# Kernel optimization log

Measured on AMD Instinct MI355X. Metric: run time of the kernel, lower is better.

Reference implementation:

```python
import jax, jax.numpy as jnp
import numpy as np

ND, NPR, DD, DP, LAT, AT, B = 2048, 2048, 128, 128, 128, 32, 16384


def setup_inputs():
    key = jax.random.key(0)
    ks = jax.random.split(key, 20)
    s = 0.05
    d = {}
    d["e_p_adj"] = (jax.random.uniform(ks[0], (ND, NPR)) < 0.05).astype(jnp.float32)
    d["e_e_adj"] = (jax.random.uniform(ks[1], (ND, ND)) < 0.05).astype(jnp.float32)
    d["p_p_adj"] = (jax.random.uniform(ks[2], (NPR, NPR)) < 0.05).astype(jnp.float32)
    d["input_disease"] = jax.random.randint(ks[3], (B,), 0, ND)
    d["input_drug"] = jax.random.randint(ks[4], (B,), 0, NPR)
    d["labels"] = jax.random.randint(ks[5], (B,), 0, 2)
    # learned parameters
    d["disease_emb"] = jax.random.normal(ks[6], (ND, DD)) * s
    d["drug_emb"] = jax.random.normal(ks[7], (NPR, DP)) * s
    d["Wdg"] = jax.random.normal(ks[8], (DP, LAT)) * s   # disease_gcn_w
    d["bdg_lin"] = jnp.zeros((LAT,))                      # Linear bias
    d["bdg"] = jnp.zeros((LAT,))                          # extra disease_gcn_b
    d["Wpg"] = jax.random.normal(ks[9], (DD, LAT)) * s   # drug_gcn_w
    d["bpg_lin"] = jnp.zeros((LAT,))
    d["bpg"] = jnp.zeros((LAT,))
    d["Wa1_d"] = jax.random.normal(ks[10], (DP + DD, AT)) * s  # concat [key(drug), query(disease)]
    d["ba1_d"] = jnp.zeros((AT,))
    d["Wa2_d"] = jax.random.normal(ks[11], (AT, 1)) * s
    d["ba2_d"] = jnp.zeros((1,))
    d["Wa1_p"] = jax.random.normal(ks[12], (DD + DP, AT)) * s  # concat [key(disease), query(drug)]
    d["ba1_p"] = jnp.zeros((AT,))
    d["Wa2_p"] = jax.random.normal(ks[13], (AT, 1)) * s
    d["ba2_p"] = jnp.zeros((1,))
    d["Wd2"] = jax.random.normal(ks[14], (DD, LAT)) * s  # disease_w2
    d["bd2"] = jnp.zeros((LAT,))
    d["Wp3"] = jax.random.normal(ks[15], (DP, LAT)) * s  # drug_w3
    d["bp3"] = jnp.zeros((LAT,))
    d["mlp_W1"] = jax.random.normal(ks[16], (LAT, DD)) * s
    d["mlp_b1"] = jnp.zeros((DD,))
    d["mlp_W2"] = jax.random.normal(ks[17], (DD, DD)) * s
    d["mlp_b2"] = jnp.zeros((DD,))
    d["Wpred"] = jax.random.normal(ks[18], (DD, 1)) * s
    d["bpred"] = jnp.zeros((1,))
    return d


def _attention_gcn(adj, other, selfe, W1, b1, W2, b2):
    # torch: concat([key=other, query=self]) -> Linear(W1) ; split W1 instead of
    # materializing the [Ns, No, Dk+Dq] concat tensor (same math, less HBM traffic)
    do = other.shape[1]
    ko = other @ W1[:do]              # [No, A]
    qs = selfe @ W1[do:]              # [Ns, A]
    h = jax.nn.relu(qs[:, None, :] + ko[None, :, :] + b1)   # [Ns, No, A]
    alpha = jax.nn.relu(jnp.squeeze(h @ W2, -1) + b2[0])    # [Ns, No]
    alpha = alpha * adj
    return jax.nn.softmax(alpha, axis=1) @ other            # [Ns, Do]


def _forward(e_p_adj, e_e_adj, p_p_adj, input_disease, input_drug, labels,
             disease_emb, drug_emb, Wdg, bdg_lin, bdg, Wpg, bpg_lin, bpg,
             Wa1_d, ba1_d, Wa2_d, ba2_d, Wa1_p, ba1_p, Wa2_p, ba2_p,
             Wd2, bd2, Wp3, bp3, mlp_W1, mlp_b1, mlp_W2, mlp_b2, Wpred, bpred):
    h_e_gcn = _attention_gcn(e_p_adj, drug_emb, disease_emb, Wa1_d, ba1_d, Wa2_d, ba2_d)
    h_e_gcn = h_e_gcn @ Wdg + bdg_lin + bdg
    h_p_gcn = _attention_gcn(e_p_adj.T, disease_emb, drug_emb, Wa1_p, ba1_p, Wa2_p, ba2_p)
    h_p_gcn = h_p_gcn @ Wpg + bpg_lin + bpg
    # disease knn branch
    deg_d = jnp.sum(e_e_adj, axis=1, keepdims=True) + 1e-8
    h_e_e = ((e_e_adj @ disease_emb) / deg_d) @ Wd2 + bd2
    h_e = jax.nn.selu(h_e_gcn + h_e_e)
    # drug knn branch
    deg_p = jnp.sum(p_p_adj, axis=1, keepdims=True) + 1e-8
    h_p_p = ((p_p_adj @ drug_emb) / deg_p) @ Wp3 + bp3
    h_p = jax.nn.selu(h_p_gcn + h_p_p)
    # pair prediction MLP
    x = h_e[input_disease] * h_p[input_drug]                # [B, LAT]
    x = jax.nn.selu(x @ mlp_W1 + mlp_b1)
    x = jax.nn.selu(x @ mlp_W2 + mlp_b2)
    z = jnp.squeeze(x @ Wpred, -1) + bpred[0]               # [B]
    y = labels.astype(jnp.float32)
    # BCEWithLogitsLoss (stable), mean reduction
    loss = jnp.mean(jnp.maximum(z, 0.0) - z * y + jnp.log1p(jnp.exp(-jnp.abs(z))))
    return (loss, jax.nn.sigmoid(z))


def reference(e_p_adj, e_e_adj, p_p_adj, input_disease, input_drug, labels,
              disease_emb, drug_emb, Wdg, bdg_lin, bdg, Wpg, bpg_lin, bpg,
              Wa1_d, ba1_d, Wa2_d, ba2_d, Wa1_p, ba1_p, Wa2_p, ba2_p,
              Wd2, bd2, Wp3, bp3, mlp_W1, mlp_b1, mlp_W2, mlp_b2, Wpred, bpred):
    return _forward(e_p_adj, e_e_adj, p_p_adj, input_disease, input_drug, labels,
                    disease_emb, drug_emb, Wdg, bdg_lin, bdg, Wpg, bpg_lin, bpg,
                    Wa1_d, ba1_d, Wa2_d, ba2_d, Wa1_p, ba1_p, Wa2_p, ba2_p,
                    Wd2, bd2, Wp3, bp3, mlp_W1, mlp_b1, mlp_W2, mlp_b2, Wpred, bpred)
```

## Files before the change

kernel.cpp:

```cpp
#include <hip/hip_runtime.h>

#define ND   2048
#define BB   16384

typedef unsigned short u16;
typedef unsigned int u32;
typedef __attribute__((ext_vector_type(8))) short short8;
typedef __attribute__((ext_vector_type(4))) float f32x4;

__device__ inline float bf2f(u16 u) {
    union { u32 i; float f; } v; v.i = ((u32)u) << 16; return v.f;
}
__device__ inline u16 f2bf(float f) {
    union { float f; u32 i; } v; v.f = f;
    u32 i = v.i + 0x7fffu + ((v.i >> 16) & 1u);
    return (u16)(i >> 16);
}
__device__ inline float seluf(float x) {
    const float sc = 1.0507009873554805f, al = 1.6732632423543772f;
    return x > 0.f ? sc * x : sc * al * expm1f(x);
}

__global__ void detectk(const void* __restrict__ demb, u32* __restrict__ flag) {
    const u16* p = (const u16*)demb;
    int tid = threadIdx.x;
    int sane = 0;
    #pragma unroll
    for (int i = 0; i < 2; i++) {
        u16 u = p[4 * tid + 2 * i];
        int e = (u >> 7) & 0xFF;
        if (u == 0 || (e >= 0x66 && e <= 0x8C)) sane++;
    }
    __shared__ int red[256];
    red[tid] = sane; __syncthreads();
    for (int o = 128; o > 0; o >>= 1) {
        if (tid < o) red[tid] += red[tid + o];
        __syncthreads();
    }
    if (tid == 0) flag[0] = (red[0] < 300) ? 1u : 0u;
}

#define NSEG 26
struct CvtArgs { const void* src[NSEG]; int off[NSEG]; int n[NSEG]; };

__global__ __launch_bounds__(256) void cvtk(CvtArgs a, u16* __restrict__ base,
                                            const u32* __restrict__ flag) {
    int seg = blockIdx.y;
    int n = a.n[seg];
    const void* s = a.src[seg];
    u16* d = base + a.off[seg];
    bool f32 = flag[0] != 0;
    int stride = gridDim.x * blockDim.x;
    for (int i = blockIdx.x * blockDim.x + threadIdx.x; i < n; i += stride)
        d[i] = f32 ? f2bf(((const float*)s)[i]) : ((const u16*)s)[i];
}

__device__ inline void tpose_body(const u16* in, int R, int C,
                                  u16* out, int ldo, int ooff,
                                  u16 (*tile)[33]) {
    int c0 = blockIdx.x * 32, r0 = blockIdx.y * 32;
    int x = c0 + threadIdx.x;
    for (int i = threadIdx.y; i < 32; i += 8) {
        int r = r0 + i;
        tile[i][threadIdx.x] = (r < R && x < C) ? in[(size_t)r * C + x] : (u16)0;
    }
    __syncthreads();
    int rr = r0 + threadIdx.x;
    for (int i = threadIdx.y; i < 32; i += 8) {
        int cc = c0 + i;
        if (cc < C && rr < R) out[(size_t)cc * ldo + ooff + rr] = tile[threadIdx.x][i];
    }
}

__global__ void tpose_smalls(const u16* s0, const u16* s1, const u16* s2,
                             const u16* s3, const u16* s4, const u16* s5,
                             u16* W1T, u16* W2T, u16* WcTe, u16* WcTp) {
    __shared__ u16 tile[32][33];
    const u16* in; u16* out; int ldo, ooff;
    switch (blockIdx.z) {
        case 0:  in = s0; out = W1T;  ldo = 128; ooff = 0;   break;
        case 1:  in = s1; out = W2T;  ldo = 128; ooff = 0;   break;
        case 2:  in = s2; out = WcTe; ldo = 256; ooff = 0;   break;
        case 3:  in = s3; out = WcTe; ldo = 256; ooff = 128; break;
        case 4:  in = s4; out = WcTp; ldo = 256; ooff = 0;   break;
        default: in = s5; out = WcTp; ldo = 256; ooff = 128; break;
    }
    tpose_body(in, 128, 128, out, ldo, ooff, tile);
}

__global__ __launch_bounds__(256) void colsump(const u16* __restrict__ demb,
                                               const u16* __restrict__ pemb,
                                               float* __restrict__ part) {
    int m = blockIdx.y;
    const u16* e = m ? pemb : demb;
    int t = threadIdx.x;
    int c2 = t & 63, rg = t >> 6;
    int r0 = blockIdx.x * 64;
    float s0 = 0.f, s1 = 0.f;
    for (int i = 0; i < 16; i++) {
        u32 v = *(const u32*)(e + (size_t)(r0 + i * 4 + rg) * 128 + c2 * 2);
        s0 += bf2f((u16)(v & 0xffffu));
        s1 += bf2f((u16)(v >> 16));
    }
    __shared__ float t0[256], t1[256];
    t0[t] = s0; t1[t] = s1;
    __syncthreads();
    if (t < 64) {
        float a0 = t0[t] + t0[t + 64] + t0[t + 128] + t0[t + 192];
        float a1 = t1[t] + t1[t + 64] + t1[t + 128] + t1[t + 192];
        part[(size_t)m * 4096 + blockIdx.x * 128 + t * 2 + 0] = a0;
        part[(size_t)m * 4096 + blockIdx.x * 128 + t * 2 + 1] = a1;
    }
}

__global__ void biasc(const u16* a0, const u16* a1, const u16* a2, u16* o0,
                      const u16* b0, const u16* b1, const u16* b2, u16* o1,
                      const float* __restrict__ part,
                      float* __restrict__ csd, float* __restrict__ csp) {
    int t = threadIdx.x;
    o0[t] = f2bf(bf2f(a0[t]) + bf2f(a1[t]) + bf2f(a2[t]));
    o1[t] = f2bf(bf2f(b0[t]) + bf2f(b1[t]) + bf2f(b2[t]));
    float sd = 0.f, sp = 0.f;
    for (int b = 0; b < 32; b++) {
        sd += part[b * 128 + t];
        sp += part[4096 + b * 128 + t];
    }
    csd[t] = sd;
    csp[t] = sp;
}

__global__ __launch_bounds__(128) void koqs(
    const u16* __restrict__ demb, const u16* __restrict__ pemb,
    const u16* __restrict__ Wa1d, const u16* __restrict__ ba1d,
    const u16* __restrict__ Wa1p, const u16* __restrict__ ba1p,
    float* __restrict__ ko_d, float* __restrict__ qs_d,
    float* __restrict__ ko_p, float* __restrict__ qs_p) {
    int row = blockIdx.x, m = blockIdx.y, tid = threadIdx.x;
    const u16* src; const u16* W; const u16* bias; float* out;
    switch (m) {
        case 0:  src = pemb; W = Wa1d;            bias = nullptr; out = ko_d; break;
        case 1:  src = demb; W = Wa1d + 128 * 32; bias = ba1d;    out = qs_d; break;
        case 2:  src = demb; W = Wa1p;            bias = nullptr; out = ko_p; break;
        default: src = pemb; W = Wa1p + 128 * 32; bias = ba1p;    out = qs_p; break;
    }
    __shared__ float x[128];
    __shared__ float red[128];
    x[tid] = bf2f(src[(size_t)row * 128 + tid]);
    __syncthreads();
    int a = tid & 31, part = tid >> 5;
    float s = 0.f;
    #pragma unroll
    for (int k = 0; k < 32; k++) s += x[part * 32 + k] * bf2f(W[(part * 32 + k) * 32 + a]);
    red[tid] = s;
    __syncthreads();
    if (part == 0) {
        float t = red[a] + red[a + 32] + red[a + 64] + red[a + 96];
        if (bias) t += bf2f(bias[a]);
        out[(size_t)row * 32 + a] = t;
    }
}

struct CS {
    const void* adj[3];
    u16* ridx[3]; u32* rcnt[3];
};

__global__ __launch_bounds__(256) void csrbuild(CS c, const u32* __restrict__ flag) {
    int m = blockIdx.y, r = blockIdx.x, t = threadIdx.x;
    int lane = t & 63;
    bool f32 = flag[0] != 0;
    __shared__ u32 lcnt;
    if (t == 0) lcnt = 0;
    __syncthreads();
    float v[8];
    int c0 = t * 8;
    if (f32) {
        const float4* p = (const float4*)((const float*)c.adj[m] + (size_t)r * 2048 + c0);
        float4 x = p[0], y = p[1];
        v[0] = x.x; v[1] = x.y; v[2] = x.z; v[3] = x.w;
        v[4] = y.x; v[5] = y.y; v[6] = y.z; v[7] = y.w;
    } else {
        const uint4* p = (const uint4*)((const u16*)c.adj[m] + (size_t)r * 2048 + c0);
        uint4 x = p[0];
        u32 u[4] = {x.x, x.y, x.z, x.w};
        #pragma unroll
        for (int i = 0; i < 4; i++) {
            v[2 * i + 0] = (u[i] & 0xffffu) ? 1.f : 0.f;
            v[2 * i + 1] = (u[i] >> 16)     ? 1.f : 0.f;
        }
    }
    int cnt = 0;
    #pragma unroll
    for (int i = 0; i < 8; i++) cnt += (v[i] != 0.f) ? 1 : 0;
    int pfx = cnt;
    #pragma unroll
    for (int o = 1; o < 64; o <<= 1) {
        int s = __shfl_up(pfx, o, 64);
        if (lane >= o) pfx += s;
    }
    int wtot = __shfl(pfx, 63, 64);
    u32 wb = 0;
    if (lane == 0) wb = atomicAdd(&lcnt, (u32)wtot);
    wb = __shfl((int)wb, 0, 64);
    int o = (int)wb + pfx - cnt;
    u16* ridx = c.ridx[m] + (size_t)r * 2048;
    #pragma unroll
    for (int i = 0; i < 8; i++) {
        if (v[i] != 0.f) ridx[o++] = (u16)(c0 + i);
    }
    __syncthreads();
    if (t == 0) c.rcnt[m][r] = lcnt;
}

__global__ __launch_bounds__(128) void colbuild(const u16* __restrict__ idx0,
                                                const u32* __restrict__ cnt0,
                                                u16* __restrict__ cidx,
                                                u32* __restrict__ ccnt) {
    int r = blockIdx.x;
    int n = (int)cnt0[r];
    const u16* row = idx0 + (size_t)r * 2048;
    for (int i = threadIdx.x; i < n; i += 128) {
        int c = (int)row[i];
        u32 q = atomicAdd(&ccnt[c], 1u);
        cidx[(size_t)c * 2048 + q] = (u16)r;
    }
}

struct SP {
    const u16* idx[4]; const u32* cnt[4];
    const float* ko[4]; const float* qs[4];
    const u16* w2[4]; const u16* b2[4];
    const u16* emb[4]; const float* csum[4];
    u16* out[4]; int ooff[4]; int attn[4];
};

__global__ __launch_bounds__(256) void spagg(SP a) {
    int task = blockIdx.y;
    int tid = threadIdx.x;
    int wv = tid >> 6, lane = tid & 63;
    int grp = lane >> 4, dim = lane & 15;
    int r = blockIdx.x * 4 + wv;
    const u16* idx = a.idx[task] + (size_t)r * 2048;
    int nnz = (int)a.cnt[task][r];
    int isat = a.attn[task];
    const u16* emb = a.emb[task];
    const float* ko = a.ko[task];

    float qsr[32], w2h[32];
    float b2v = 0.f;
    if (isat) {
        const float4* qp = (const float4*)(a.qs[task] + (size_t)r * 32);
        #pragma unroll
        for (int i = 0; i < 8; i++) {
            float4 v = qp[i];
            qsr[4 * i + 0] = v.x; qsr[4 * i + 1] = v.y;
            qsr[4 * i + 2] = v.z; qsr[4 * i + 3] = v.w;
        }
        #pragma unroll
        for (int i = 0; i < 32; i++) w2h[i] = bf2f(a.w2[task][i]);
        b2v = bf2f(a.b2[task][0]);
    }

    float acc[8];
    #pragma unroll
    for (int t = 0; t < 8; t++) acc[t] = 0.f;
    float wsuml = 0.f;

    for (int base = 0; base < nnz; base += 64) {
        int i = base + lane;
        float w = 0.f;
        int j = 0;
        if (i < nnz) {
            j = (int)idx[i];
            if (isat) {
                const float4* kp = (const float4*)(ko + (size_t)j * 32);
                float s = 0.f;
                #pragma unroll
                for (int q = 0; q < 8; q++) {
                    float4 kv = kp[q];
                    s += fmaxf(qsr[4 * q + 0] + kv.x, 0.f) * w2h[4 * q + 0];
                    s += fmaxf(qsr[4 * q + 1] + kv.y, 0.f) * w2h[4 * q + 1];
                    s += fmaxf(qsr[4 * q + 2] + kv.z, 0.f) * w2h[4 * q + 2];
                    s += fmaxf(qsr[4 * q + 3] + kv.w, 0.f) * w2h[4 * q + 3];
                }
                w = __expf(fmaxf(s + b2v, 0.f)) - 1.f;
            } else {
                w = 1.f;
            }
        }
        wsuml += w;
        int cend = min(64, nnz - base);
        #pragma unroll 4
        for (int k4 = 0; k4 < cend; k4 += 4) {
            int kk = k4 + grp;
            float wk = __shfl(w, kk, 64);
            int jk = __shfl(j, kk, 64);
            const uint4* p = (const uint4*)((const char*)emb + jk * 256 + dim * 16);
            uint4 vv = *p;
            u32 u[4] = {vv.x, vv.y, vv.z, vv.w};
            #pragma unroll
            for (int cc = 0; cc < 4; cc++) {
                acc[2 * cc + 0] = fmaf(wk, bf2f((u16)(u[cc] & 0xffffu)), acc[2 * cc + 0]);
                acc[2 * cc + 1] = fmaf(wk, bf2f((u16)(u[cc] >> 16)), acc[2 * cc + 1]);
            }
        }
    }

    #pragma unroll
    for (int t = 0; t < 8; t++) {
        acc[t] += __shfl_xor(acc[t], 32, 64);
        acc[t] += __shfl_xor(acc[t], 16, 64);
    }
    #pragma unroll
    for (int o = 32; o > 0; o >>= 1) wsuml += __shfl_xor(wsuml, o, 64);

    if (grp == 0) {
        float v[8];
        if (isat) {
            float sc = 1.f / (2048.f + wsuml);
            const float* cs = a.csum[task] + dim * 8;
            #pragma unroll
            for (int t = 0; t < 8; t++) v[t] = (cs[t] + acc[t]) * sc;
        } else {
            float sc = 1.f / (wsuml + 1e-8f);
            #pragma unroll
            for (int t = 0; t < 8; t++) v[t] = acc[t] * sc;
        }
        uint4 pk;
        pk.x = (u32)f2bf(v[0]) | ((u32)f2bf(v[1]) << 16);
        pk.y = (u32)f2bf(v[2]) | ((u32)f2bf(v[3]) << 16);
        pk.z = (u32)f2bf(v[4]) | ((u32)f2bf(v[5]) << 16);
        pk.w = (u32)f2bf(v[6]) | ((u32)f2bf(v[7]) << 16);
        *(uint4*)(a.out[task] + (size_t)r * 256 + a.ooff[task] + dim * 8) = pk;
    }
}

struct GD4 {
    const void* A[4]; const u16* BT[4]; u16* C[4];
    const u16* bias[4]; const float* rs[4];
    int lda[4], ldb[4], ldc[4], coff[4], kiters[4], act[4], araw[4], rsmode[4];
};

#define PADK 136

__global__ __launch_bounds__(256, 2) void gemmL(GD4 g, const u32* __restrict__ flag) {
    __shared__ __align__(16) u16 As[16][PADK];
    __shared__ __align__(16) u16 Bs[128][PADK];
    int z = blockIdx.y;
    const void* A = g.A[z];
    const u16* BT = g.BT[z];
    int lda = g.lda[z], ldb = g.ldb[z];
    int kiters = g.kiters[z];
    int tid = threadIdx.x;
    int lane = tid & 63, wv = tid >> 6;
    int mrow = lane & 15, quad = lane >> 4;
    int m0 = blockIdx.x * 16;
    int c0 = wv * 32;
    int sr = tid >> 4, sk = (tid & 15) * 8;
    f32x4 acc0 = {0.f, 0.f, 0.f, 0.f}, acc1 = {0.f, 0.f, 0.f, 0.f};

    short8 ra, rb[8];
    auto ldstage = [&](int kb) {
        ra = *(const short8*)((const u16*)A + (size_t)(m0 + sr) * lda + kb + sk);
        const u16* bbase = BT + (size_t)sr * ldb + kb + sk;
        #pragma unroll
        for (int i = 0; i < 8; i++)
            rb[i] = *(const short8*)(bbase + (size_t)i * 16 * ldb);
    };
    auto ststage = [&]() {
        *(short8*)(&As[sr][sk]) = ra;
        #pragma unroll
        for (int i = 0; i < 8; i++)
            *(short8*)(&Bs[i * 16 + sr][sk]) = rb[i];
    };
    auto compute = [&]() {
        #pragma unroll
        for (int ks = 0; ks < 4; ks++) {
            short8 af = *(const short8*)(&As[mrow][ks * 32 + quad * 8]);
            short8 b0 = *(const short8*)(&Bs[c0 + mrow][ks * 32 + quad * 8]);
            short8 b1 = *(const short8*)(&Bs[c0 + 16 + mrow][ks * 32 + quad * 8]);
            acc0 = __builtin_amdgcn_mfma_f32_16x16x32_bf16(af, b0, acc0, 0, 0, 0);
            acc1 = __builtin_amdgcn_mfma_f32_16x16x32_bf16(af, b1, acc1, 0, 0, 0);
        }
    };

    ldstage(0);
    #pragma unroll 1
    for (int it = 0; it < kiters - 1; ++it) {
        ststage();
        __syncthreads();
        ldstage((it + 1) * 128);
        compute();
        __syncthreads();
    }
    ststage();
    __syncthreads();
    compute();

    const float* rs = g.rs[z];
    int rsmode = g.rsmode[z];
    const u16* bi = g.bias[z];
    u16* C = g.C[z];
    int ldc = g.ldc[z], coff = g.coff[z], act = g.act[z];
    int n0 = c0 + mrow, n1 = n0 + 16;
    float bv0 = bi ? bf2f(bi[n0]) : 0.f;
    float bv1 = bi ? bf2f(bi[n1]) : 0.f;
    #pragma unroll
    for (int r = 0; r < 4; r++) {
        int row = m0 + quad * 4 + r;
        float v0 = acc0[r], v1 = acc1[r];
        if (rsmode == 1) { float sc = rs[row]; v0 *= sc; v1 *= sc; }
        else if (rsmode == 2) {
            float t = 0.f;
            #pragma unroll
            for (int p = 0; p < 8; p++) t += rs[row + p * 2048];
            float sc = 1.f / t;
            v0 *= sc; v1 *= sc;
        }
        v0 += bv0; v1 += bv1;
        if (act) { v0 = seluf(v0); v1 = seluf(v1); }
        C[(size_t)row * ldc + coff + n0] = f2bf(v0);
        C[(size_t)row * ldc + coff + n1] = f2bf(v1);
    }
}

#define PADX 136
__global__ __launch_bounds__(256, 2) void mlpfused(
    const u16* __restrict__ he, const u16* __restrict__ hp,
    const int* __restrict__ di, const int* __restrict__ dr,
    const u16* __restrict__ W1T, const u16* __restrict__ b1,
    const u16* __restrict__ W2T, const u16* __restrict__ b2,
    const u16* __restrict__ wpred, const u16* __restrict__ bpred,
    const int* __restrict__ labels,
    float* __restrict__ out, float* __restrict__ part) {
    __shared__ __align__(16) u16 Xs[64][PADX];
    __shared__ __align__(16) u16 Ws[128][PADX];
    __shared__ float wred[4];
    int tid = threadIdx.x;
    int lane = tid & 63, wv = tid >> 6;
    int mrow = lane & 15, quad = lane >> 4;
    int p0 = blockIdx.x * 64;

    {
        int row = tid >> 2, sub = tid & 3;
        int b = p0 + row;
        int ia = di[b], ic = dr[b];
        const uint4* pe = (const uint4*)(he + (size_t)ia * 128 + sub * 32);
        const uint4* pp = (const uint4*)(hp + (size_t)ic * 128 + sub * 32);
        #pragma unroll
        for (int q = 0; q < 4; q++) {
            uint4 ue = pe[q], up = pp[q];
            u32 eu[4] = {ue.x, ue.y, ue.z, ue.w};
            u32 pu[4] = {up.x, up.y, up.z, up.w};
            #pragma unroll
            for (int c = 0; c < 4; c++) {
                float lo = bf2f((u16)(eu[c] & 0xffffu)) * bf2f((u16)(pu[c] & 0xffffu));
                float hi = bf2f((u16)(eu[c] >> 16)) * bf2f((u16)(pu[c] >> 16));
                *(u32*)(&Xs[row][sub * 32 + q * 8 + c * 2]) =
                    (u32)f2bf(lo) | ((u32)f2bf(hi) << 16);
            }
        }
    }
    {
        int n = tid >> 1, half = tid & 1;
        const short8* src = (const short8*)(W1T + (size_t)n * 128 + half * 64);
        short8* dst = (short8*)(&Ws[n][half * 64]);
        #pragma unroll
        for (int i = 0; i < 8; i++) dst[i] = src[i];
    }
    __syncthreads();

    f32x4 acc[8];
    #pragma unroll
    for (int nt = 0; nt < 8; nt++) acc[nt] = {0.f, 0.f, 0.f, 0.f};
    #pragma unroll
    for (int ks = 0; ks < 4; ks++) {
        short8 af = *(const short8*)(&Xs[wv * 16 + mrow][ks * 32 + quad * 8]);
        #pragma unroll
        for (int nt = 0; nt < 8; nt++) {
            short8 bfv = *(const short8*)(&Ws[nt * 16 + mrow][ks * 32 + quad * 8]);
            acc[nt] = __builtin_amdgcn_mfma_f32_16x16x32_bf16(af, bfv, acc[nt], 0, 0, 0);
        }
    }
    __syncthreads();
    #pragma unroll
    for (int nt = 0; nt < 8; nt++) {
        int col = nt * 16 + mrow;
        float bv = bf2f(b1[col]);
        #pragma unroll
        for (int r = 0; r < 4; r++) {
            int row = wv * 16 + quad * 4 + r;
            Xs[row][col] = f2bf(seluf(acc[nt][r] + bv));
        }
    }
    {
        int n = tid >> 1, half = tid & 1;
        const short8* src = (const short8*)(W2T + (size_t)n * 128 + half * 64);
        short8* dst = (short8*)(&Ws[n][half * 64]);
        #pragma unroll
        for (int i = 0; i < 8; i++) dst[i] = src[i];
    }
    __syncthreads();

    #pragma unroll
    for (int nt = 0; nt < 8; nt++) acc[nt] = {0.f, 0.f, 0.f, 0.f};
    #pragma unroll
    for (int ks = 0; ks < 4; ks++) {
        short8 af = *(const short8*)(&Xs[wv * 16 + mrow][ks * 32 + quad * 8]);
        #pragma unroll
        for (int nt = 0; nt < 8; nt++) {
            short8 bfv = *(const short8*)(&Ws[nt * 16 + mrow][ks * 32 + quad * 8]);
            acc[nt] = __builtin_amdgcn_mfma_f32_16x16x32_bf16(af, bfv, acc[nt], 0, 0, 0);
        }
    }

    float zp[4] = {0.f, 0.f, 0.f, 0.f};
    #pragma unroll
    for (int nt = 0; nt < 8; nt++) {
        int col = nt * 16 + mrow;
        float bv = bf2f(b2[col]);
        float wp = bf2f(wpred[col]);
        #pragma unroll
        for (int r = 0; r < 4; r++) {
            float x2 = bf2f(f2bf(seluf(acc[nt][r] + bv)));
            zp[r] = fmaf(x2, wp, zp[r]);
        }
    }
    #pragma unroll
    for (int r = 0; r < 4; r++) {
        #pragma unroll
        for (int o = 1; o < 16; o <<= 1) zp[r] += __shfl_xor(zp[r], o, 64);
    }
    float bpv = bf2f(bpred[0]);
    float lsum = 0.f;
    #pragma unroll
    for (int r = 0; r < 4; r++) {
        int b = p0 + wv * 16 + quad * 4 + r;
        float z = zp[r] + bpv;
        float sig = 1.f / (1.f + __expf(-z));
        if (mrow == 0) out[1 + b] = sig;
        float y = (float)labels[b];
        lsum += fmaxf(z, 0.f) - z * y + log1pf(__expf(-fabsf(z)));
    }
    lsum += __shfl_xor(lsum, 16, 64);
    lsum += __shfl_xor(lsum, 32, 64);
    if (lane == 0) wred[wv] = lsum;
    __syncthreads();
    if (tid == 0) part[blockIdx.x] = wred[0] + wred[1] + wred[2] + wred[3];
}

__global__ void finloss(const float* __restrict__ part, float* __restrict__ out) {
    __shared__ float s[256];
    int t = threadIdx.x;
    s[t] = part[t];
    __syncthreads();
    for (int o = 128; o > 0; o >>= 1) {
        if (t < o) s[t] += s[t + o];
        __syncthreads();
    }
    if (t == 0) out[0] = s[0] * (1.f / 16384.f);
}

extern "C" void kernel_launch(void* const* d_in, const int* in_sizes, int n_in,
                              void* d_out, int out_size, void* d_ws, size_t ws_size,
                              hipStream_t stream) {
    const void* e_p_adj = d_in[0];
    const void* e_e_adj = d_in[1];
    const void* p_p_adj = d_in[2];
    const int* in_dis  = (const int*)d_in[3];
    const int* in_drug = (const int*)d_in[4];
    const int* labels  = (const int*)d_in[5];
    float* out = (float*)d_out;

    char* ws = (char*)d_ws;
    size_t off = 0;
    auto take = [&](size_t bytes) { char* p = ws + off; off = (off + bytes + 255) & ~(size_t)255; return p; };
    u16*   A_e   = (u16*)take((size_t)2048 * 256 * 2);
    u16*   A_p   = (u16*)take((size_t)2048 * 256 * 2);
    u16*   WcTe  = (u16*)take((size_t)128 * 256 * 2);
    u16*   WcTp  = (u16*)take((size_t)128 * 256 * 2);
    u16*   W1T   = (u16*)take((size_t)128 * 128 * 2);
    u16*   W2T   = (u16*)take((size_t)128 * 128 * 2);
    u16*   b_e   = (u16*)take(256);
    u16*   b_p   = (u16*)take(256);
    u16*   h_e   = (u16*)take((size_t)2048 * 128 * 2);
    u16*   h_p   = (u16*)take((size_t)2048 * 128 * 2);
    float* ko_d  = (float*)take((size_t)2048 * 32 * 4);
    float* qs_d  = (float*)take((size_t)2048 * 32 * 4);
    float* ko_p  = (float*)take((size_t)2048 * 32 * 4);
    float* qs_p  = (float*)take((size_t)2048 * 32 * 4);
    float* cspart = (float*)take((size_t)2 * 32 * 128 * 4);
    float* csd   = (float*)take(128 * 4);
    float* csp   = (float*)take(128 * 4);
    float* part  = (float*)take(256 * 4);
    u32*   flag  = (u32*)take(256);
    u16*   canon = (u16*)take((size_t)700000 * 2);
    u16*   idx0  = (u16*)take((size_t)2048 * 2048 * 2);
    u16*   idx1  = (u16*)take((size_t)2048 * 2048 * 2);
    u16*   idx2  = (u16*)take((size_t)2048 * 2048 * 2);
    u16*   idx3  = (u16*)take((size_t)2048 * 2048 * 2);
    u32*   cnt0  = (u32*)take(2048 * 4);
    u32*   cnt2  = (u32*)take(2048 * 4);
    u32*   cnt3  = (u32*)take(2048 * 4);
    u32*   cntT  = (u32*)take(2048 * 4);

    const int segidx[NSEG] = {6, 7, 14, 18, 8, 22, 11, 24, 26, 28,
                              15, 16, 17, 19, 20, 21,
                              9, 10, 12, 13, 23, 25, 27, 29, 30, 31};
    const int segn[NSEG]   = {262144, 262144, 8192, 8192, 16384, 16384, 16384, 16384, 16384, 16384,
                              32, 32, 1, 32, 32, 1,
                              128, 128, 128, 128, 128, 128, 128, 128, 128, 1};
    CvtArgs ca;
    u16* cp[NSEG];
    {
        int o = 0;
        for (int i = 0; i < NSEG; i++) {
            ca.src[i] = d_in[segidx[i]];
            ca.off[i] = o;
            ca.n[i] = segn[i];
            cp[i] = canon + o;
            o += (segn[i] + 15) & ~15;
        }
    }
    u16 *cdemb = cp[0], *cpemb = cp[1], *cWa1d = cp[2], *cWa1p = cp[3];
    u16 *cWdg = cp[4], *cWd2 = cp[5], *cWpg = cp[6], *cWp3 = cp[7];
    u16 *cW1 = cp[8], *cW2 = cp[9];
    u16 *cba1d = cp[10], *cWa2d = cp[11], *cba2d = cp[12];
    u16 *cba1p = cp[13], *cWa2p = cp[14], *cba2p = cp[15];
    u16 *cbdg_lin = cp[16], *cbdg = cp[17], *cbpg_lin = cp[18], *cbpg = cp[19];
    u16 *cbd2 = cp[20], *cbp3 = cp[21], *cmb1 = cp[22], *cmb2 = cp[23];
    u16 *cWpred = cp[24], *cbpred = cp[25];

    detectk<<<1, 256, 0, stream>>>(d_in[6], flag);
    cvtk<<<dim3(64, NSEG), 256, 0, stream>>>(ca, canon, flag);

    hipMemsetAsync(cntT, 0, 2048 * sizeof(u32), stream);
    {
        CS cs;
        cs.adj[0] = e_p_adj; cs.ridx[0] = idx0; cs.rcnt[0] = cnt0;
        cs.adj[1] = e_e_adj; cs.ridx[1] = idx2; cs.rcnt[1] = cnt2;
        cs.adj[2] = p_p_adj; cs.ridx[2] = idx3; cs.rcnt[2] = cnt3;
        csrbuild<<<dim3(2048, 3), 256, 0, stream>>>(cs, flag);
    }
    colbuild<<<2048, 128, 0, stream>>>(idx0, cnt0, idx1, cntT);

    colsump<<<dim3(32, 2), 256, 0, stream>>>(cdemb, cpemb, cspart);
    tpose_smalls<<<dim3(4, 4, 6), dim3(32, 8), 0, stream>>>(
        cW1, cW2, cWdg, cWd2, cWpg, cWp3, W1T, W2T, WcTe, WcTp);
    biasc<<<1, 128, 0, stream>>>(cbdg_lin, cbdg, cbd2, b_e, cbpg_lin, cbpg, cbp3, b_p,
                                 cspart, csd, csp);
    koqs<<<dim3(2048, 4), 128, 0, stream>>>(cdemb, cpemb, cWa1d, cba1d, cWa1p, cba1p,
                                            ko_d, qs_d, ko_p, qs_p);

    {
        SP sp;
        sp.idx[0] = idx0; sp.cnt[0] = cnt0; sp.ko[0] = ko_d; sp.qs[0] = qs_d;
        sp.w2[0] = cWa2d; sp.b2[0] = cba2d; sp.emb[0] = cpemb; sp.csum[0] = csp;
        sp.out[0] = A_e; sp.ooff[0] = 0; sp.attn[0] = 1;
        sp.idx[1] = idx2; sp.cnt[1] = cnt2; sp.ko[1] = ko_d; sp.qs[1] = qs_d;
        sp.w2[1] = cWa2d; sp.b2[1] = cba2d; sp.emb[1] = cdemb; sp.csum[1] = csd;
        sp.out[1] = A_e; sp.ooff[1] = 128; sp.attn[1] = 0;
        sp.idx[2] = idx1; sp.cnt[2] = cntT; sp.ko[2] = ko_p; sp.qs[2] = qs_p;
        sp.w2[2] = cWa2p; sp.b2[2] = cba2p; sp.emb[2] = cdemb; sp.csum[2] = csd;
        sp.out[2] = A_p; sp.ooff[2] = 0; sp.attn[2] = 1;
        sp.idx[3] = idx3; sp.cnt[3] = cnt3; sp.ko[3] = ko_p; sp.qs[3] = qs_p;
        sp.w2[3] = cWa2p; sp.b2[3] = cba2p; sp.emb[3] = cpemb; sp.csum[3] = csp;
        sp.out[3] = A_p; sp.ooff[3] = 128; sp.attn[3] = 0;
        spagg<<<dim3(512, 4), 256, 0, stream>>>(sp);
    }

    auto setd = [](GD4& g, int z, const void* A, int lda, const u16* BT, int ldb,
                   u16* C, int ldc, int coff, int ki, const u16* bi,
                   const float* rs, int act, int araw, int rm) {
        g.A[z] = A; g.lda[z] = lda; g.BT[z] = BT; g.ldb[z] = ldb;
        g.C[z] = C; g.ldc[z] = ldc; g.coff[z] = coff; g.kiters[z] = ki;
        g.bias[z] = bi; g.rs[z] = rs; g.act[z] = act; g.araw[z] = araw; g.rsmode[z] = rm;
    };

    {
        GD4 g;
        setd(g, 0, A_e, 256, WcTe, 256, h_e, 128, 0, 2, b_e, nullptr, 1, 0, 0);
        setd(g, 1, A_p, 256, WcTp, 256, h_p, 128, 0, 2, b_p, nullptr, 1, 0, 0);
        setd(g, 2, A_e, 256, WcTe, 256, h_e, 128, 0, 2, b_e, nullptr, 1, 0, 0);
        setd(g, 3, A_e, 256, WcTe, 256, h_e, 128, 0, 2, b_e, nullptr, 1, 0, 0);
        gemmL<<<dim3(128, 2), 256, 0, stream>>>(g, flag);
    }

    mlpfused<<<256, 256, 0, stream>>>(h_e, h_p, in_dis, in_drug,
                                      W1T, cmb1, W2T, cmb2,
                                      cWpred, cbpred, labels, out, part);
    finloss<<<1, 256, 0, stream>>>(part, out);
}
```

Before: 242.6 us.

## Fuse preprocessing kernels into combined launches and skip weights for plain mean aggregation

Merges dtype conversion and CSR building into one launch, and merges koqs, column-CSR build, weight transposes and column sums into a single multi-role kernel. The memset is folded into detectk. This cuts the number of small sequential launches. In the non-attention spagg path, per-edge weights are replaced by a mask and the normaliser by nnz, which drops a shuffle reduction. The fused blocks raise shared-memory use per block, and the cvt segment now runs in the same launch as csrbuild.

```diff
diff --git a/kernel.cpp b/kernel.cpp
--- a/kernel.cpp
+++ b/kernel.cpp
@@ -21,9 +21,12 @@
     return x > 0.f ? sc * x : sc * al * expm1f(x);
 }
 
-__global__ void detectk(const void* __restrict__ demb, u32* __restrict__ flag) {
+__global__ void detectk(const void* __restrict__ demb, u32* __restrict__ flag,
+                        u32* __restrict__ cntT) {
     const u16* p = (const u16*)demb;
     int tid = threadIdx.x;
+    #pragma unroll
+    for (int i = 0; i < 8; i++) cntT[i * 256 + tid] = 0u;
     int sane = 0;
     #pragma unroll
     for (int i = 0; i < 2; i++) {
@@ -42,188 +45,182 @@
 
 #define NSEG 26
 struct CvtArgs { const void* src[NSEG]; int off[NSEG]; int n[NSEG]; };
-
-__global__ __launch_bounds__(256) void cvtk(CvtArgs a, u16* __restrict__ base,
-                                            const u32* __restrict__ flag) {
-    int seg = blockIdx.y;
-    int n = a.n[seg];
-    const void* s = a.src[seg];
-    u16* d = base + a.off[seg];
-    bool f32 = flag[0] != 0;
-    int stride = gridDim.x * blockDim.x;
-    for (int i = blockIdx.x * blockDim.x + threadIdx.x; i < n; i += stride)
-        d[i] = f32 ? f2bf(((const float*)s)[i]) : ((const u16*)s)[i];
-}
-
-__device__ inline void tpose_body(const u16* in, int R, int C,
-                                  u16* out, int ldo, int ooff,
-                                  u16 (*tile)[33]) {
-    int c0 = blockIdx.x * 32, r0 = blockIdx.y * 32;
-    int x = c0 + threadIdx.x;
-    for (int i = threadIdx.y; i < 32; i += 8) {
-        int r = r0 + i;
-        tile[i][threadIdx.x] = (r < R && x < C) ? in[(size_t)r * C + x] : (u16)0;
-    }
-    __syncthreads();
-    int rr = r0 + threadIdx.x;
-    for (int i = threadIdx.y; i < 32; i += 8) {
-        int cc = c0 + i;
-        if (cc < C && rr < R) out[(size_t)cc * ldo + ooff + rr] = tile[threadIdx.x][i];
-    }
-}
-
-__global__ void tpose_smalls(const u16* s0, const u16* s1, const u16* s2,
-                             const u16* s3, const u16* s4, const u16* s5,
-                             u16* W1T, u16* W2T, u16* WcTe, u16* WcTp) {
-    __shared__ u16 tile[32][33];
-    const u16* in; u16* out; int ldo, ooff;
-    switch (blockIdx.z) {
-        case 0:  in = s0; out = W1T;  ldo = 128; ooff = 0;   break;
-        case 1:  in = s1; out = W2T;  ldo = 128; ooff = 0;   break;
-        case 2:  in = s2; out = WcTe; ldo = 256; ooff = 0;   break;
-        case 3:  in = s3; out = WcTe; ldo = 256; ooff = 128; break;
-        case 4:  in = s4; out = WcTp; ldo = 256; ooff = 0;   break;
-        default: in = s5; out = WcTp; ldo = 256; ooff = 128; break;
-    }
-    tpose_body(in, 128, 128, out, ldo, ooff, tile);
-}
-
-__global__ __launch_bounds__(256) void colsump(const u16* __restrict__ demb,
-                                               const u16* __restrict__ pemb,
-                                               float* __restrict__ part) {
-    int m = blockIdx.y;
-    const u16* e = m ? pemb : demb;
-    int t = threadIdx.x;
-    int c2 = t & 63, rg = t >> 6;
-    int r0 = blockIdx.x * 64;
-    float s0 = 0.f, s1 = 0.f;
-    for (int i = 0; i < 16; i++) {
-        u32 v = *(const u32*)(e + (size_t)(r0 + i * 4 + rg) * 128 + c2 * 2);
-        s0 += bf2f((u16)(v & 0xffffu));
-        s1 += bf2f((u16)(v >> 16));
-    }
-    __shared__ float t0[256], t1[256];
-    t0[t] = s0; t1[t] = s1;
-    __syncthreads();
-    if (t < 64) {
-        float a0 = t0[t] + t0[t + 64] + t0[t + 128] + t0[t + 192];
-        float a1 = t1[t] + t1[t + 64] + t1[t + 128] + t1[t + 192];
-        part[(size_t)m * 4096 + blockIdx.x * 128 + t * 2 + 0] = a0;
-        part[(size_t)m * 4096 + blockIdx.x * 128 + t * 2 + 1] = a1;
-    }
-}
-
-__global__ void biasc(const u16* a0, const u16* a1, const u16* a2, u16* o0,
-                      const u16* b0, const u16* b1, const u16* b2, u16* o1,
-                      const float* __restrict__ part,
-                      float* __restrict__ csd, float* __restrict__ csp) {
-    int t = threadIdx.x;
-    o0[t] = f2bf(bf2f(a0[t]) + bf2f(a1[t]) + bf2f(a2[t]));
-    o1[t] = f2bf(bf2f(b0[t]) + bf2f(b1[t]) + bf2f(b2[t]));
-    float sd = 0.f, sp = 0.f;
-    for (int b = 0; b < 32; b++) {
-        sd += part[b * 128 + t];
-        sp += part[4096 + b * 128 + t];
-    }
-    csd[t] = sd;
-    csp[t] = sp;
-}
-
-__global__ __launch_bounds__(128) void koqs(
-    const u16* __restrict__ demb, const u16* __restrict__ pemb,
-    const u16* __restrict__ Wa1d, const u16* __restrict__ ba1d,
-    const u16* __restrict__ Wa1p, const u16* __restrict__ ba1p,
-    float* __restrict__ ko_d, float* __restrict__ qs_d,
-    float* __restrict__ ko_p, float* __restrict__ qs_p) {
-    int row = blockIdx.x, m = blockIdx.y, tid = threadIdx.x;
-    const u16* src; const u16* W; const u16* bias; float* out;
-    switch (m) {
-        case 0:  src = pemb; W = Wa1d;            bias = nullptr; out = ko_d; break;
-        case 1:  src = demb; W = Wa1d + 128 * 32; bias = ba1d;    out = qs_d; break;
-        case 2:  src = demb; W = Wa1p;            bias = nullptr; out = ko_p; break;
-        default: src = pemb; W = Wa1p + 128 * 32; bias = ba1p;    out = qs_p; break;
-    }
-    __shared__ float x[128];
-    __shared__ float red[128];
-    x[tid] = bf2f(src[(size_t)row * 128 + tid]);
-    __syncthreads();
-    int a = tid & 31, part = tid >> 5;
-    float s = 0.f;
-    #pragma unroll
-    for (int k = 0; k < 32; k++) s += x[part * 32 + k] * bf2f(W[(part * 32 + k) * 32 + a]);
-    red[tid] = s;
-    __syncthreads();
-    if (part == 0) {
-        float t = red[a] + red[a + 32] + red[a + 64] + red[a + 96];
-        if (bias) t += bf2f(bias[a]);
-        out[(size_t)row * 32 + a] = t;
-    }
-}
-
 struct CS {
     const void* adj[3];
     u16* ridx[3]; u32* rcnt[3];
 };
 
-__global__ __launch_bounds__(256) void csrbuild(CS c, const u32* __restrict__ flag) {
-    int m = blockIdx.y, r = blockIdx.x, t = threadIdx.x;
-    int lane = t & 63;
+__global__ __launch_bounds__(256) void cvtcsr(CvtArgs a, u16* __restrict__ base,
+                                              CS c, const u32* __restrict__ flag) {
+    int bx = blockIdx.x;
+    int t = threadIdx.x;
     bool f32 = flag[0] != 0;
-    __shared__ u32 lcnt;
-    if (t == 0) lcnt = 0;
-    __syncthreads();
-    float v[8];
-    int c0 = t * 8;
-    if (f32) {
-        const float4* p = (const float4*)((const float*)c.adj[m] + (size_t)r * 2048 + c0);
-        float4 x = p[0], y = p[1];
-        v[0] = x.x; v[1] = x.y; v[2] = x.z; v[3] = x.w;
-        v[4] = y.x; v[5] = y.y; v[6] = y.z; v[7] = y.w;
+    if (bx < 6144) {
+        int m = bx >> 11, r = bx & 2047;
+        int lane = t & 63;
+        __shared__ u32 lcnt;
+        if (t == 0) lcnt = 0;
+        __syncthreads();
+        float v[8];
+        int c0 = t * 8;
+        if (f32) {
+            const float4* p = (const float4*)((const float*)c.adj[m] + (size_t)r * 2048 + c0);
+            float4 x = p[0], y = p[1];
+            v[0] = x.x; v[1] = x.y; v[2] = x.z; v[3] = x.w;
+            v[4] = y.x; v[5] = y.y; v[6] = y.z; v[7] = y.w;
+        } else {
+            const uint4* p = (const uint4*)((const u16*)c.adj[m] + (size_t)r * 2048 + c0);
+            uint4 x = p[0];
+            u32 u[4] = {x.x, x.y, x.z, x.w};
+            #pragma unroll
+            for (int i = 0; i < 4; i++) {
+                v[2 * i + 0] = (u[i] & 0xffffu) ? 1.f : 0.f;
+                v[2 * i + 1] = (u[i] >> 16)     ? 1.f : 0.f;
+            }
+        }
+        int cnt = 0;
+        #pragma unroll
+        for (int i = 0; i < 8; i++) cnt += (v[i] != 0.f) ? 1 : 0;
+        int pfx = cnt;
+        #pragma unroll
+        for (int o = 1; o < 64; o <<= 1) {
+            int s = __shfl_up(pfx, o, 64);
+            if (lane >= o) pfx += s;
+        }
+        int wtot = __shfl(pfx, 63, 64);
+        u32 wb = 0;
+        if (lane == 0) wb = atomicAdd(&lcnt, (u32)wtot);
+        wb = __shfl((int)wb, 0, 64);
+        int o = (int)wb + pfx - cnt;
+        u16* ridx = c.ridx[m] + (size_t)r * 2048;
+        #pragma unroll
+        for (int i = 0; i < 8; i++) {
+            if (v[i] != 0.f) ridx[o++] = (u16)(c0 + i);
+        }
+        __syncthreads();
+        if (t == 0) c.rcnt[m][r] = lcnt;
     } else {
-        const uint4* p = (const uint4*)((const u16*)c.adj[m] + (size_t)r * 2048 + c0);
-        uint4 x = p[0];
-        u32 u[4] = {x.x, x.y, x.z, x.w};
-        #pragma unroll
-        for (int i = 0; i < 4; i++) {
-            v[2 * i + 0] = (u[i] & 0xffffu) ? 1.f : 0.f;
-            v[2 * i + 1] = (u[i] >> 16)     ? 1.f : 0.f;
-        }
-    }
-    int cnt = 0;
-    #pragma unroll
-    for (int i = 0; i < 8; i++) cnt += (v[i] != 0.f) ? 1 : 0;
-    int pfx = cnt;
-    #pragma unroll
-    for (int o = 1; o < 64; o <<= 1) {
-        int s = __shfl_up(pfx, o, 64);
-        if (lane >= o) pfx += s;
-    }
-    int wtot = __shfl(pfx, 63, 64);
-    u32 wb = 0;
-    if (lane == 0) wb = atomicAdd(&lcnt, (u32)wtot);
-    wb = __shfl((int)wb, 0, 64);
-    int o = (int)wb + pfx - cnt;
-    u16* ridx = c.ridx[m] + (size_t)r * 2048;
-    #pragma unroll
-    for (int i = 0; i < 8; i++) {
-        if (v[i] != 0.f) ridx[o++] = (u16)(c0 + i);
-    }
-    __syncthreads();
-    if (t == 0) c.rcnt[m][r] = lcnt;
-}
-
-__global__ __launch_bounds__(128) void colbuild(const u16* __restrict__ idx0,
-                                                const u32* __restrict__ cnt0,
-                                                u16* __restrict__ cidx,
-                                                u32* __restrict__ ccnt) {
-    int r = blockIdx.x;
-    int n = (int)cnt0[r];
-    const u16* row = idx0 + (size_t)r * 2048;
-    for (int i = threadIdx.x; i < n; i += 128) {
-        int c = (int)row[i];
-        u32 q = atomicAdd(&ccnt[c], 1u);
-        cidx[(size_t)c * 2048 + q] = (u16)r;
-    }
+        int idx = bx - 6144;
+        int seg = idx >> 6, xb = idx & 63;
+        int n = a.n[seg];
+        const void* s = a.src[seg];
+        u16* d = base + a.off[seg];
+        for (int i = xb * 256 + t; i < n; i += 16384)
+            d[i] = f32 ? f2bf(((const float*)s)[i]) : ((const u16*)s)[i];
+    }
+}
+
+struct PR {
+    const u16* demb; const u16* pemb;
+    const u16* Wa1d; const u16* ba1d;
+    const u16* Wa1p; const u16* ba1p;
+    float* ko_d; float* qs_d; float* ko_p; float* qs_p;
+    const u16* idx0; const u32* cnt0; u16* cidx; u32* ccnt;
+    const u16* ts[6]; u16* W1T; u16* W2T; u16* WcTe; u16* WcTp;
+    float* cspart;
+    const u16* ba[3]; const u16* bb[3]; u16* b_e; u16* b_p;
+    float* csd; float* csp;
+};
+
+__global__ __launch_bounds__(256) void prep2(PR p) {
+    int bx = blockIdx.x;
+    int tid = threadIdx.x;
+    __shared__ float sx[2][128];
+    __shared__ float sred[2][128];
+    __shared__ u16 stile[32][33];
+    __shared__ float st0[256], st1[256];
+
+    if (bx < 4096) {
+        int sub = tid >> 7, t = tid & 127;
+        int unit = bx * 2 + sub;
+        int row = unit & 2047, m = unit >> 11;
+        const u16* src; const u16* W; const u16* bias; float* out;
+        switch (m) {
+            case 0:  src = p.pemb; W = p.Wa1d;            bias = nullptr; out = p.ko_d; break;
+            case 1:  src = p.demb; W = p.Wa1d + 128 * 32; bias = p.ba1d;  out = p.qs_d; break;
+            case 2:  src = p.demb; W = p.Wa1p;            bias = nullptr; out = p.ko_p; break;
+            default: src = p.pemb; W = p.Wa1p + 128 * 32; bias = p.ba1p;  out = p.qs_p; break;
+        }
+        sx[sub][t] = bf2f(src[(size_t)row * 128 + t]);
+        __syncthreads();
+        int a = t & 31, part = t >> 5;
+        float s = 0.f;
+        #pragma unroll
+        for (int k = 0; k < 32; k++)
+            s += sx[sub][part * 32 + k] * bf2f(W[(part * 32 + k) * 32 + a]);
+        sred[sub][t] = s;
+        __syncthreads();
+        if (part == 0) {
+            float tt = sred[sub][a] + sred[sub][a + 32] + sred[sub][a + 64] + sred[sub][a + 96];
+            if (bias) tt += bf2f(bias[a]);
+            out[(size_t)row * 32 + a] = tt;
+        }
+    } else if (bx < 6144) {
+        int r = bx - 4096;
+        int n = (int)p.cnt0[r];
+        const u16* row = p.idx0 + (size_t)r * 2048;
+        for (int i = tid; i < n; i += 256) {
+            int cc = (int)row[i];
+            u32 q = atomicAdd(&p.ccnt[cc], 1u);
+            p.cidx[(size_t)cc * 2048 + q] = (u16)r;
+        }
+    } else if (bx < 6240) {
+        int id = bx - 6144;
+        int z = id >> 4, rem = id & 15;
+        int c0 = (rem & 3) * 32, r0 = (rem >> 2) * 32;
+        const u16* in = p.ts[z];
+        u16* out; int ldo, ooff;
+        switch (z) {
+            case 0:  out = p.W1T;  ldo = 128; ooff = 0;   break;
+            case 1:  out = p.W2T;  ldo = 128; ooff = 0;   break;
+            case 2:  out = p.WcTe; ldo = 256; ooff = 0;   break;
+            case 3:  out = p.WcTe; ldo = 256; ooff = 128; break;
+            case 4:  out = p.WcTp; ldo = 256; ooff = 0;   break;
+            default: out = p.WcTp; ldo = 256; ooff = 128; break;
+        }
+        int tx = tid & 31, ty = tid >> 5;
+        int x = c0 + tx;
+        for (int i = ty; i < 32; i += 8)
+            stile[i][tx] = in[(size_t)(r0 + i) * 128 + x];
+        __syncthreads();
+        int rr = r0 + tx;
+        for (int i = ty; i < 32; i += 8)
+            out[(size_t)(c0 + i) * ldo + ooff + rr] = stile[tx][i];
+    } else if (bx < 6304) {
+        int id = bx - 6240;
+        int m = id >> 5, xb = id & 31;
+        const u16* e = m ? p.pemb : p.demb;
+        int c2 = tid & 63, rg = tid >> 6;
+        int r0 = xb * 64;
+        float s0 = 0.f, s1 = 0.f;
+        for (int i = 0; i < 16; i++) {
+            u32 v = *(const u32*)(e + (size_t)(r0 + i * 4 + rg) * 128 + c2 * 2);
+            s0 += bf2f((u16)(v & 0xffffu));
+            s1 += bf2f((u16)(v >> 16));
+        }
+        st0[tid] = s0; st1[tid] = s1;
+        __syncthreads();
+        if (tid < 64) {
+            float a0 = st0[tid] + st0[tid + 64] + st0[tid + 128] + st0[tid + 192];
+            float a1 = st1[tid] + st1[tid + 64] + st1[tid + 128] + st1[tid + 192];
+            p.cspart[(size_t)m * 4096 + xb * 128 + tid * 2 + 0] = a0;
+            p.cspart[(size_t)m * 4096 + xb * 128 + tid * 2 + 1] = a1;
+        }
+    } else {
+    }
+}
+
+__global__ void biasfin(PR p) {
+    int t = threadIdx.x;
+    p.b_e[t] = f2bf(bf2f(p.ba[0][t]) + bf2f(p.ba[1][t]) + bf2f(p.ba[2][t]));
+    p.b_p[t] = f2bf(bf2f(p.bb[0][t]) + bf2f(p.bb[1][t]) + bf2f(p.bb[2][t]));
+    float sd = 0.f, sp = 0.f;
+    for (int b = 0; b < 32; b++) {
+        sd += p.cspart[b * 128 + t];
+        sp += p.cspart[4096 + b * 128 + t];
+    }
+    p.csd[t] = sd;
+    p.csp[t] = sp;
 }
 
 struct SP {
@@ -284,19 +281,18 @@
                     s += fmaxf(qsr[4 * q + 3] + kv.w, 0.f) * w2h[4 * q + 3];
                 }
                 w = __expf(fmaxf(s + b2v, 0.f)) - 1.f;
-            } else {
-                w = 1.f;
+                wsuml += w;
             }
         }
-        wsuml += w;
         int cend = min(64, nnz - base);
         #pragma unroll 4
         for (int k4 = 0; k4 < cend; k4 += 4) {
             int kk = k4 + grp;
-            float wk = __shfl(w, kk, 64);
             int jk = __shfl(j, kk, 64);
-            const uint4* p = (const uint4*)((const char*)emb + jk * 256 + dim * 16);
-            uint4 vv = *p;
+            float wk = isat ? __shfl(w, kk, 64)
+                            : ((base + kk < nnz) ? 1.f : 0.f);
+            const uint4* pp = (const uint4*)((const char*)emb + jk * 256 + dim * 16);
+            uint4 vv = *pp;
             u32 u[4] = {vv.x, vv.y, vv.z, vv.w};
             #pragma unroll
             for (int cc = 0; cc < 4; cc++) {
@@ -311,8 +307,10 @@
         acc[t] += __shfl_xor(acc[t], 32, 64);
         acc[t] += __shfl_xor(acc[t], 16, 64);
     }
-    #pragma unroll
-    for (int o = 32; o > 0; o >>= 1) wsuml += __shfl_xor(wsuml, o, 64);
+    if (isat) {
+        #pragma unroll
+        for (int o = 32; o > 0; o >>= 1) wsuml += __shfl_xor(wsuml, o, 64);
+    }
 
     if (grp == 0) {
         float v[8];
@@ -322,7 +320,7 @@
             #pragma unroll
             for (int t = 0; t < 8; t++) v[t] = (cs[t] + acc[t]) * sc;
         } else {
-            float sc = 1.f / (wsuml + 1e-8f);
+            float sc = 1.f / ((float)nnz + 1e-8f);
             #pragma unroll
             for (int t = 0; t < 8; t++) v[t] = acc[t] * sc;
         }
@@ -631,26 +629,30 @@
     u16 *cbd2 = cp[20], *cbp3 = cp[21], *cmb1 = cp[22], *cmb2 = cp[23];
     u16 *cWpred = cp[24], *cbpred = cp[25];
 
-    detectk<<<1, 256, 0, stream>>>(d_in[6], flag);
-    cvtk<<<dim3(64, NSEG), 256, 0, stream>>>(ca, canon, flag);
-
-    hipMemsetAsync(cntT, 0, 2048 * sizeof(u32), stream);
+    detectk<<<1, 256, 0, stream>>>(d_in[6], flag, cntT);
+
     {
         CS cs;
         cs.adj[0] = e_p_adj; cs.ridx[0] = idx0; cs.rcnt[0] = cnt0;
         cs.adj[1] = e_e_adj; cs.ridx[1] = idx2; cs.rcnt[1] = cnt2;
         cs.adj[2] = p_p_adj; cs.ridx[2] = idx3; cs.rcnt[2] = cnt3;
-        csrbuild<<<dim3(2048, 3), 256, 0, stream>>>(cs, flag);
-    }
-    colbuild<<<2048, 128, 0, stream>>>(idx0, cnt0, idx1, cntT);
-
-    colsump<<<dim3(32, 2), 256, 0, stream>>>(cdemb, cpemb, cspart);
-    tpose_smalls<<<dim3(4, 4, 6), dim3(32, 8), 0, stream>>>(
-        cW1, cW2, cWdg, cWd2, cWpg, cWp3, W1T, W2T, WcTe, WcTp);
-    biasc<<<1, 128, 0, stream>>>(cbdg_lin, cbdg, cbd2, b_e, cbpg_lin, cbpg, cbp3, b_p,
-                                 cspart, csd, csp);
-    koqs<<<dim3(2048, 4), 128, 0, stream>>>(cdemb, cpemb, cWa1d, cba1d, cWa1p, cba1p,
-                                            ko_d, qs_d, ko_p, qs_p);
+        cvtcsr<<<6144 + 64 * NSEG, 256, 0, stream>>>(ca, canon, cs, flag);
+    }
+
+    PR pr;
+    pr.demb = cdemb; pr.pemb = cpemb;
+    pr.Wa1d = cWa1d; pr.ba1d = cba1d; pr.Wa1p = cWa1p; pr.ba1p = cba1p;
+    pr.ko_d = ko_d; pr.qs_d = qs_d; pr.ko_p = ko_p; pr.qs_p = qs_p;
+    pr.idx0 = idx0; pr.cnt0 = cnt0; pr.cidx = idx1; pr.ccnt = cntT;
+    pr.ts[0] = cW1; pr.ts[1] = cW2; pr.ts[2] = cWdg;
+    pr.ts[3] = cWd2; pr.ts[4] = cWpg; pr.ts[5] = cWp3;
+    pr.W1T = W1T; pr.W2T = W2T; pr.WcTe = WcTe; pr.WcTp = WcTp;
+    pr.cspart = cspart;
+    pr.ba[0] = cbdg_lin; pr.ba[1] = cbdg; pr.ba[2] = cbd2;
+    pr.bb[0] = cbpg_lin; pr.bb[1] = cbpg; pr.bb[2] = cbp3;
+    pr.b_e = b_e; pr.b_p = b_p; pr.csd = csd; pr.csp = csp;
+    prep2<<<6304, 256, 0, stream>>>(pr);
+    biasfin<<<1, 128, 0, stream>>>(pr);
 
     {
         SP sp;
```

Result: faster. 236.5 us (-2.5%).
